# Kernel tuning notes

Measured on AMD Instinct MI355X. Metric: run time of the kernel, lower is better.

The kernel has to match this reference:

```python
import jax, jax.numpy as jnp
import numpy as np

B, S, H = 1, 2048, 2048
NH, NKV, HD = 16, 4, 128
LAT, RD = 512, 64
ND = HD - RD  # nope_dim = 64
EPS = 1e-6


def _rms(x, g):
    return x * jax.lax.rsqrt(jnp.mean(x * x, axis=-1, keepdims=True) + EPS) * g


def _rotate_half(x):
    x1, x2 = jnp.split(x, 2, axis=-1)
    return jnp.concatenate([-x2, x1], axis=-1)


def _rope(x, cos, sin):
    # x: [B,S,nh,RD]; cos/sin: [S,RD] -> broadcast over batch and heads
    c = cos[None, :, None, :]
    s = sin[None, :, None, :]
    return x * c + _rotate_half(x) * s


def setup_inputs() -> dict:
    key = jax.random.key(0)
    ks = jax.random.split(key, 10)
    x = jax.random.normal(ks[0], (B, S, H), jnp.float32)
    # rotary tables (theta=10000) for rope_dim
    inv = 1.0 / (10000.0 ** (np.arange(0, RD, 2, dtype=np.float32) / RD))
    t = np.arange(S, dtype=np.float32)
    freqs = np.outer(t, inv)  # [S, RD/2]
    emb = np.concatenate([freqs, freqs], axis=-1)  # [S, RD]
    cos = jnp.asarray(np.cos(emb), jnp.float32)
    sin = jnp.asarray(np.sin(emb), jnp.float32)
    sc = lambda fan_in: 1.0 / np.sqrt(fan_in)
    Wq_nope = jax.random.normal(ks[1], (NH * ND, H), jnp.float32) * sc(H)
    Wq_rope = jax.random.normal(ks[2], (NH * RD, H), jnp.float32) * sc(H)
    W_kv_down = jax.random.normal(ks[3], (LAT, H), jnp.float32) * sc(H)
    W_k_nope = jax.random.normal(ks[4], (NKV * ND, LAT), jnp.float32) * sc(LAT)
    W_k_rope = jax.random.normal(ks[5], (NKV * RD, LAT), jnp.float32) * sc(LAT)
    W_v = jax.random.normal(ks[6], (NKV * HD, LAT), jnp.float32) * sc(LAT)
    W_o = jax.random.normal(ks[7], (H, NH * HD), jnp.float32) * sc(NH * HD)
    return {
        "x": x, "cos": cos, "sin": sin,
        "Wq_nope": Wq_nope, "Wq_rope": Wq_rope,
        "g_qnope": jnp.ones((ND,), jnp.float32),
        "g_qrope": jnp.ones((RD,), jnp.float32),
        "W_kv_down": W_kv_down, "g_ckv": jnp.ones((LAT,), jnp.float32),
        "W_k_nope": W_k_nope, "W_k_rope": W_k_rope,
        "W_v": W_v, "W_o": W_o,
    }


def reference(x, cos, sin, Wq_nope, Wq_rope, g_qnope, g_qrope,
              W_kv_down, g_ckv, W_k_nope, W_k_rope, W_v, W_o):
    n_rep = NH // NKV
    # queries: decoupled nope / rope parts, RMSNorm each, RoPE on rope part
    q_nope = _rms((x @ Wq_nope.T).reshape(B, S, NH, ND), g_qnope)
    q_rope = _rms((x @ Wq_rope.T).reshape(B, S, NH, RD), g_qrope)
    q_rope = _rope(q_rope, cos[:S, :RD], sin[:S, :RD])
    q = jnp.concatenate([q_nope, q_rope], axis=-1)  # [B,S,NH,HD]
    # latent KV compression
    c_kv = _rms(x @ W_kv_down.T, g_ckv)  # [B,S,LAT]
    k_nope = (c_kv @ W_k_nope.T).reshape(B, S, NKV, ND)
    k_rope = _rope((c_kv @ W_k_rope.T).reshape(B, S, NKV, RD), cos[:S, :RD], sin[:S, :RD])
    v = (c_kv @ W_v.T).reshape(B, S, NKV, HD)
    k = jnp.concatenate([k_nope, k_rope], axis=-1)  # [B,S,NKV,HD]
    # repeat kv heads
    k = jnp.repeat(k, n_rep, axis=2)  # [B,S,NH,HD]
    v = jnp.repeat(v, n_rep, axis=2)
    # causal attention, softmax in fp32
    scores = jnp.einsum("bqhd,bkhd->bhqk", q, k) / jnp.sqrt(jnp.asarray(HD, jnp.float32))
    causal = jnp.tril(jnp.ones((S, S), bool))
    scores = jnp.where(causal[None, None], scores, -jnp.inf)
    attn = jax.nn.softmax(scores.astype(jnp.float32), axis=-1).astype(q.dtype)
    out = jnp.einsum("bhqk,bkhd->bqhd", attn, v).reshape(B, S, NH * HD)
    return out @ W_o.T  # [B,S,H]
```

## Files before the change

### kernel.cpp

```cpp
#include <hip/hip_runtime.h>
#include <hip/hip_bf16.h>
#include <math.h>

#define TPB 256

typedef __attribute__((ext_vector_type(8))) short bf16x8;
typedef __attribute__((ext_vector_type(4))) float f32x4;

__device__ __forceinline__ short f2bs(float x) {
  __hip_bfloat16 h = __float2bfloat16(x);
  return *reinterpret_cast<short*>(&h);
}

__device__ __forceinline__ void gll16(const void* g, void* l) {
  __builtin_amdgcn_global_load_lds(
      (const __attribute__((address_space(1))) unsigned int*)g,
      (__attribute__((address_space(3))) unsigned int*)l, 16, 0, 0);
}

__global__ __launch_bounds__(TPB) void cvt_f2b(
    const float* __restrict__ s, short* __restrict__ d, int n)
{
  int i = (blockIdx.x * TPB + threadIdx.x) << 2;
  if (i >= n) return;
  const float4 v = *(const float4*)(s + i);
  short4 o;
  o.x = f2bs(v.x); o.y = f2bs(v.y); o.z = f2bs(v.z); o.w = f2bs(v.w);
  *(short4*)(d + i) = o;
}

__global__ __launch_bounds__(TPB) void cvt_weights(
    const float* __restrict__ w0, const float* __restrict__ w1,
    const float* __restrict__ w2, const float* __restrict__ w3,
    const float* __restrict__ w4, const float* __restrict__ w5,
    const float* __restrict__ w6,
    short* __restrict__ Wcat, short* __restrict__ Wkvb, short* __restrict__ Wob)
{
  int b = blockIdx.x;
  const float* src; short* dst; int base;
  if (b < 2048)      { src = w0; dst = Wcat;           base = b; }
  else if (b < 4096) { src = w1; dst = Wcat + 2097152; base = b - 2048; }
  else if (b < 5120) { src = w2; dst = Wcat + 4194304; base = b - 4096; }
  else if (b < 5248) { src = w3; dst = Wkvb;           base = b - 5120; }
  else if (b < 5376) { src = w4; dst = Wkvb + 131072;  base = b - 5248; }
  else if (b < 5632) { src = w5; dst = Wkvb + 262144;  base = b - 5376; }
  else               { src = w6; dst = Wob;            base = b - 5632; }
  int i = base * 1024 + threadIdx.x * 4;
  float4 v = *(const float4*)(src + i);
  short4 o;
  o.x = f2bs(v.x); o.y = f2bs(v.y); o.z = f2bs(v.z); o.w = f2bs(v.w);
  *(short4*)(dst + i) = o;
}

__global__ __launch_bounds__(TPB) void rms512b(
    const float* __restrict__ src, short* __restrict__ dst,
    const float* __restrict__ g, int nrows)
{
  int row = blockIdx.x * (TPB / 64) + (threadIdx.x >> 6);
  int l = threadIdx.x & 63;
  if (row >= nrows) return;
  const float* p = src + (size_t)row * 512;
  float x[8];
  float ss = 0.f;
#pragma unroll
  for (int i = 0; i < 8; ++i) { x[i] = p[i * 64 + l]; ss += x[i] * x[i]; }
#pragma unroll
  for (int msk = 1; msk < 64; msk <<= 1) ss += __shfl_xor(ss, msk);
  float r = rsqrtf(ss * (1.0f / 512.0f) + 1e-6f);
#pragma unroll
  for (int i = 0; i < 8; ++i)
    dst[(size_t)row * 512 + i * 64 + l] = f2bs(x[i] * r * g[i * 64 + l]);
}

template <int MODE>
__global__ __launch_bounds__(TPB) void gemm_fused(
    const short* __restrict__ A, const short* __restrict__ W,
    float* __restrict__ Cf, short* __restrict__ qk_out, short* __restrict__ vt,
    float* __restrict__ ckv_f,
    const float* __restrict__ cosb, const float* __restrict__ sinb,
    const float* __restrict__ g_qnope, const float* __restrict__ g_qrope,
    int M, int N, int K, int ldc)
{
  __shared__ short As[2][128 * 64];
  __shared__ short Bs[2][128 * 64];
  const int t = threadIdx.x;
  const int lane = t & 63, wave = t >> 6;
  const int wr = wave >> 1, wc = wave & 1;
  const int li = lane & 15, lh = lane >> 4;
  const int bm = blockIdx.y * 128, bn = blockIdx.x * 128;

  f32x4 acc[4][4];
#pragma unroll
  for (int m = 0; m < 4; ++m)
#pragma unroll
    for (int n = 0; n < 4; ++n) acc[m][n] = (f32x4){0.f, 0.f, 0.f, 0.f};

#define GSTAGE(buf, k0)                                                        \
  {                                                                            \
    _Pragma("unroll") for (int i = 0; i < 4; ++i) {                            \
      int id = i * 256 + t;                                                    \
      int r = id >> 3, cl = id & 7;                                            \
      gll16(A + (size_t)(bm + r) * K + (k0) + ((cl ^ (r & 7)) << 3),           \
            &As[buf][id * 8]);                                                 \
    }                                                                          \
    _Pragma("unroll") for (int i = 0; i < 4; ++i) {                            \
      int id = i * 256 + t;                                                    \
      int r = id >> 3, cl = id & 7;                                            \
      gll16(W + (size_t)(bn + r) * K + (k0) + ((cl ^ (r & 7)) << 3),           \
            &Bs[buf][id * 8]);                                                 \
    }                                                                          \
  }

  GSTAGE(0, 0);
  int cur = 0;
  for (int k0 = 0; k0 < K; k0 += 64) {
    __builtin_amdgcn_sched_barrier(0);
    asm volatile("s_waitcnt lgkmcnt(0)" ::: "memory");
    __builtin_amdgcn_s_barrier();
    __builtin_amdgcn_sched_barrier(0);
    if (k0 + 64 < K) {
      GSTAGE(cur ^ 1, k0 + 64);
      asm volatile("s_waitcnt vmcnt(8)" ::: "memory");
    } else {
      asm volatile("s_waitcnt vmcnt(0)" ::: "memory");
    }
    __builtin_amdgcn_sched_barrier(0);
    bf16x8 af[2][4], bf[2][4];
#pragma unroll
    for (int m = 0; m < 4; ++m) {
      int r = wr * 64 + m * 16 + li;
#pragma unroll
      for (int kd = 0; kd < 2; ++kd)
        af[kd][m] = *(const bf16x8*)&As[cur][r * 64 + (((kd * 4 + lh) ^ (r & 7)) << 3)];
    }
#pragma unroll
    for (int n = 0; n < 4; ++n) {
      int r = wc * 64 + n * 16 + li;
#pragma unroll
      for (int kd = 0; kd < 2; ++kd)
        bf[kd][n] = *(const bf16x8*)&Bs[cur][r * 64 + (((kd * 4 + lh) ^ (r & 7)) << 3)];
    }
    __builtin_amdgcn_s_setprio(1);
#pragma unroll
    for (int kd = 0; kd < 2; ++kd)
#pragma unroll
      for (int m = 0; m < 4; ++m)
#pragma unroll
        for (int n = 0; n < 4; ++n)
          acc[m][n] = __builtin_amdgcn_mfma_f32_16x16x32_bf16(af[kd][m], bf[kd][n],
                                                              acc[m][n], 0, 0, 0);
    __builtin_amdgcn_s_setprio(0);
    __builtin_amdgcn_sched_barrier(0);
    cur ^= 1;
  }
#undef GSTAGE

  const int colbase = bn + wc * 64;

  if (MODE == 0) {
#pragma unroll
    for (int m = 0; m < 4; ++m) {
      int gm = bm + wr * 64 + m * 16 + lh * 4;
#pragma unroll
      for (int n = 0; n < 4; ++n) {
        int gn = colbase + n * 16 + li;
#pragma unroll
        for (int j = 0; j < 4; ++j)
          Cf[(size_t)(gm + j) * ldc + gn] = acc[m][n][j];
      }
    }
  }

  if (MODE == 1) {
    if (colbase < 2048) {
      const bool isrope = colbase >= 1024;
      const int head = (colbase & 1023) >> 6;
      const float* g = isrope ? g_qrope : g_qnope;
      float gv[4];
#pragma unroll
      for (int nf = 0; nf < 4; ++nf) gv[nf] = g[nf * 16 + li];
#pragma unroll
      for (int m = 0; m < 4; ++m) {
#pragma unroll
        for (int j = 0; j < 4; ++j) {
          int s = bm + wr * 64 + m * 16 + lh * 4 + j;
          float sum = acc[m][0][j] * acc[m][0][j] + acc[m][1][j] * acc[m][1][j] +
                      acc[m][2][j] * acc[m][2][j] + acc[m][3][j] * acc[m][3][j];
          sum += __shfl_xor(sum, 1); sum += __shfl_xor(sum, 2);
          sum += __shfl_xor(sum, 4); sum += __shfl_xor(sum, 8);
          float r = rsqrtf(sum * (1.0f / 64.0f) + 1e-6f);
          float y[4];
#pragma unroll
          for (int nf = 0; nf < 4; ++nf) y[nf] = acc[m][nf][j] * r * gv[nf];
          if (isrope) {
            float yr[4];
#pragma unroll
            for (int nf = 0; nf < 4; ++nf) {
              int c = nf * 16 + li;
              float cs = cosb[s * 64 + c], sn = sinb[s * 64 + c];
              float par = (nf < 2) ? -y[nf + 2] : y[nf - 2];
              yr[nf] = y[nf] * cs + par * sn;
            }
#pragma unroll
            for (int nf = 0; nf < 4; ++nf) y[nf] = yr[nf];
          }
#pragma unroll
          for (int nf = 0; nf < 4; ++nf)
            qk_out[(size_t)s * 2048 + head * 128 + (isrope ? 64 : 0) + nf * 16 + li] =
                f2bs(y[nf]);
        }
      }
    } else {
      const int c0 = colbase - 2048;
#pragma unroll
      for (int m = 0; m < 4; ++m) {
        int gm = bm + wr * 64 + m * 16 + lh * 4;
#pragma unroll
        for (int n = 0; n < 4; ++n) {
          int c = c0 + n * 16 + li;
#pragma unroll
          for (int j = 0; j < 4; ++j)
            ckv_f[(size_t)(gm + j) * 512 + c] = acc[m][n][j];
        }
      }
    }
  }

  if (MODE == 2) {
    if (colbase < 512) {
      const bool isrope = colbase >= 256;
      const int kvh = (colbase & 255) >> 6;
#pragma unroll
      for (int m = 0; m < 4; ++m) {
#pragma unroll
        for (int j = 0; j < 4; ++j) {
          int s = bm + wr * 64 + m * 16 + lh * 4 + j;
          float y[4];
#pragma unroll
          for (int nf = 0; nf < 4; ++nf) y[nf] = acc[m][nf][j];
          if (isrope) {
            float yr[4];
#pragma unroll
            for (int nf = 0; nf < 4; ++nf) {
              int c = nf * 16 + li;
              float cs = cosb[s * 64 + c], sn = sinb[s * 64 + c];
              float par = (nf < 2) ? -y[nf + 2] : y[nf - 2];
              yr[nf] = y[nf] * cs + par * sn;
            }
#pragma unroll
            for (int nf = 0; nf < 4; ++nf) y[nf] = yr[nf];
          }
#pragma unroll
          for (int nf = 0; nf < 4; ++nf)
            qk_out[(size_t)s * 512 + kvh * 128 + (isrope ? 64 : 0) + nf * 16 + li] =
                f2bs(y[nf]);
        }
      }
    } else {
#pragma unroll
      for (int m = 0; m < 4; ++m) {
        int s0 = bm + wr * 64 + m * 16 + lh * 4;
#pragma unroll
        for (int nf = 0; nf < 4; ++nf) {
          int d = colbase - 512 + nf * 16 + li;
          int kvh = d >> 7, dd = d & 127;
          short4 pk;
          pk.x = f2bs(acc[m][nf][0]); pk.y = f2bs(acc[m][nf][1]);
          pk.z = f2bs(acc[m][nf][2]); pk.w = f2bs(acc[m][nf][3]);
          *(short4*)&vt[(size_t)kvh * 262144 + (size_t)dd * 2048 + s0] = pk;
        }
      }
    }
  }
}

__global__ __launch_bounds__(TPB) void attn_mfma(
    const short* __restrict__ qb, const short* __restrict__ kb,
    const short* __restrict__ vt, short* __restrict__ ob)
{
  __shared__ short Ks[2][64 * 128];
  __shared__ short Vs[2][128 * 64];
  __shared__ short Ps[4][16 * 64];
  const int h = blockIdx.x;
  const int qt = gridDim.y - 1 - blockIdx.y;
  const int kvh = h >> 2;
  const int t = threadIdx.x, lane = t & 63, wave = t >> 6;
  const int li = lane & 15, lh = lane >> 4;
  const int q0 = qt * 64, q0w = q0 + wave * 16;
  const float scale = 0.08838834764831845f;

  bf16x8 qf[4];
#pragma unroll
  for (int kd = 0; kd < 4; ++kd)
    qf[kd] = *(const bf16x8*)(qb + (size_t)(q0w + li) * 2048 + h * 128 + kd * 32 + lh * 8);

  f32x4 o[8];
#pragma unroll
  for (int n = 0; n < 8; ++n) o[n] = (f32x4){0.f, 0.f, 0.f, 0.f};
  float m_i[4] = {-1e30f, -1e30f, -1e30f, -1e30f};
  float l_i[4] = {0.f, 0.f, 0.f, 0.f};

#define ASTAGE(buf, kbase)                                                     \
  {                                                                            \
    _Pragma("unroll") for (int i = 0; i < 4; ++i) {                            \
      int c = t + i * 256;                                                     \
      int kpos = c >> 4, dcl = (c & 15) ^ (kpos & 7);                          \
      gll16(kb + (size_t)((kbase) + kpos) * 512 + kvh * 128 + dcl * 8,         \
            &Ks[buf][c * 8]);                                                  \
    }                                                                          \
    _Pragma("unroll") for (int i = 0; i < 4; ++i) {                            \
      int c = t + i * 256;                                                     \
      int d = c >> 3, kpl = (c & 7) ^ (d & 7);                                 \
      gll16(vt + (size_t)kvh * 262144 + (size_t)d * 2048 + (kbase) + kpl * 8,  \
            &Vs[buf][c * 8]);                                                  \
    }                                                                          \
  }

  short* pw = Ps[wave];
  const int nkt = qt + 1;
  ASTAGE(0, 0);
  int cur = 0;
  for (int kt = 0; kt < nkt; ++kt) {
    const int kbase = kt * 64;
    __builtin_amdgcn_sched_barrier(0);
    asm volatile("s_waitcnt lgkmcnt(0)" ::: "memory");
    __builtin_amdgcn_s_barrier();
    __builtin_amdgcn_sched_barrier(0);
    if (kt + 1 < nkt) {
      ASTAGE(cur ^ 1, kbase + 64);
      asm volatile("s_waitcnt vmcnt(8)" ::: "memory");
    } else {
      asm volatile("s_waitcnt vmcnt(0)" ::: "memory");
    }
    __builtin_amdgcn_sched_barrier(0);

    f32x4 s[4];
#pragma unroll
    for (int n = 0; n < 4; ++n) s[n] = (f32x4){0.f, 0.f, 0.f, 0.f};
    __builtin_amdgcn_s_setprio(1);
#pragma unroll
    for (int n = 0; n < 4; ++n) {
      int kpos = n * 16 + li;
#pragma unroll
      for (int kd = 0; kd < 4; ++kd) {
        int cph = (kd * 4 + lh) ^ (kpos & 7);
        bf16x8 kf = *(const bf16x8*)&Ks[cur][kpos * 128 + cph * 8];
        s[n] = __builtin_amdgcn_mfma_f32_16x16x32_bf16(qf[kd], kf, s[n], 0, 0, 0);
      }
    }
    __builtin_amdgcn_s_setprio(0);
    float sv[4][4];
    const bool diag = (kt == nkt - 1);
#pragma unroll
    for (int n = 0; n < 4; ++n)
#pragma unroll
      for (int j = 0; j < 4; ++j) {
        float val = s[n][j] * scale;
        if (diag) {
          int kg = kbase + n * 16 + li;
          int qg = q0w + lh * 4 + j;
          if (kg > qg) val = -1e30f;
        }
        sv[n][j] = val;
      }
    float c_[4];
#pragma unroll
    for (int j = 0; j < 4; ++j) {
      float rm = fmaxf(fmaxf(sv[0][j], sv[1][j]), fmaxf(sv[2][j], sv[3][j]));
      rm = fmaxf(rm, __shfl_xor(rm, 1));
      rm = fmaxf(rm, __shfl_xor(rm, 2));
      rm = fmaxf(rm, __shfl_xor(rm, 4));
      rm = fmaxf(rm, __shfl_xor(rm, 8));
      float mn = fmaxf(m_i[j], rm);
      c_[j] = __expf(m_i[j] - mn);
      m_i[j] = mn;
    }
#pragma unroll
    for (int n = 0; n < 4; ++n)
#pragma unroll
      for (int j = 0; j < 4; ++j) sv[n][j] = __expf(sv[n][j] - m_i[j]);
#pragma unroll
    for (int j = 0; j < 4; ++j) {
      float rs = sv[0][j] + sv[1][j] + sv[2][j] + sv[3][j];
      rs += __shfl_xor(rs, 1);
      rs += __shfl_xor(rs, 2);
      rs += __shfl_xor(rs, 4);
      rs += __shfl_xor(rs, 8);
      l_i[j] = l_i[j] * c_[j] + rs;
    }
#pragma unroll
    for (int n = 0; n < 4; ++n)
#pragma unroll
      for (int j = 0; j < 4; ++j) {
        int qq = lh * 4 + j, kp = n * 16 + li;
        pw[qq * 64 + (kp ^ ((qq & 7) << 3))] = f2bs(sv[n][j]);
      }
    if (__any((c_[0] < 1.f) | (c_[1] < 1.f) | (c_[2] < 1.f) | (c_[3] < 1.f))) {
#pragma unroll
      for (int n = 0; n < 8; ++n)
#pragma unroll
        for (int j = 0; j < 4; ++j) o[n][j] *= c_[j];
    }
    asm volatile("s_waitcnt lgkmcnt(0)" ::: "memory");
    __builtin_amdgcn_sched_barrier(0);
    __builtin_amdgcn_s_setprio(1);
#pragma unroll
    for (int kk = 0; kk < 2; ++kk) {
      int kp0 = kk * 32 + lh * 8;
      bf16x8 pf = *(const bf16x8*)&pw[li * 64 + (kp0 ^ ((li & 7) << 3))];
#pragma unroll
      for (int n = 0; n < 8; ++n) {
        int d = n * 16 + li;
        bf16x8 vf = *(const bf16x8*)&Vs[cur][d * 64 + (kp0 ^ ((d & 7) << 3))];
        o[n] = __builtin_amdgcn_mfma_f32_16x16x32_bf16(pf, vf, o[n], 0, 0, 0);
      }
    }
    __builtin_amdgcn_s_setprio(0);
    __builtin_amdgcn_sched_barrier(0);
    cur ^= 1;
  }
#undef ASTAGE
  float inv[4];
#pragma unroll
  for (int j = 0; j < 4; ++j) inv[j] = 1.0f / l_i[j];
#pragma unroll
  for (int n = 0; n < 8; ++n)
#pragma unroll
    for (int j = 0; j < 4; ++j)
      ob[(size_t)(q0w + lh * 4 + j) * 2048 + h * 128 + n * 16 + li] =
          f2bs(o[n][j] * inv[j]);
}

extern "C" void kernel_launch(void* const* d_in, const int* in_sizes, int n_in,
                              void* d_out, int out_size, void* d_ws, size_t ws_size,
                              hipStream_t stream) {
  const float* x         = (const float*)d_in[0];
  const float* cosb      = (const float*)d_in[1];
  const float* sinb      = (const float*)d_in[2];
  const float* Wq_nope   = (const float*)d_in[3];
  const float* Wq_rope   = (const float*)d_in[4];
  const float* g_qnope   = (const float*)d_in[5];
  const float* g_qrope   = (const float*)d_in[6];
  const float* W_kv_down = (const float*)d_in[7];
  const float* g_ckv     = (const float*)d_in[8];
  const float* W_k_nope  = (const float*)d_in[9];
  const float* W_k_rope  = (const float*)d_in[10];
  const float* W_v       = (const float*)d_in[11];
  const float* W_o       = (const float*)d_in[12];
  float* out = (float*)d_out;

  float* ws = (float*)d_ws;
  float* ckv_f = ws;
  short* sb   = (short*)(ws + 1048576);
  short* xb   = sb;
  short* Wcat = sb + 4194304;
  short* Wkvb = Wcat + 5242880;
  short* Wob  = Wkvb + 524288;
  short* qb   = Wob + 4194304;
  short* ckvb = qb + 4194304;
  short* kb   = ckvb + 1048576;
  short* vt   = kb + 1048576;
  short* aob  = xb;

  dim3 blk(TPB);

  cvt_f2b<<<4096, blk, 0, stream>>>(x, xb, 4194304);
  cvt_weights<<<9728, blk, 0, stream>>>(Wq_nope, Wq_rope, W_kv_down, W_k_nope,
                                        W_k_rope, W_v, W_o, Wcat, Wkvb, Wob);

  gemm_fused<1><<<dim3(20, 16), blk, 0, stream>>>(
      xb, Wcat, nullptr, qb, nullptr, ckv_f, cosb, sinb, g_qnope, g_qrope,
      2048, 2560, 2048, 0);

  rms512b<<<512, blk, 0, stream>>>(ckv_f, ckvb, g_ckv, 2048);

  gemm_fused<2><<<dim3(8, 16), blk, 0, stream>>>(
      ckvb, Wkvb, nullptr, kb, vt, nullptr, cosb, sinb, nullptr, nullptr,
      2048, 1024, 512, 0);

  attn_mfma<<<dim3(16, 32), blk, 0, stream>>>(qb, kb, vt, aob);

  gemm_fused<0><<<dim3(16, 16), blk, 0, stream>>>(
      aob, Wob, out, nullptr, nullptr, nullptr, nullptr, nullptr, nullptr, nullptr,
      2048, 2048, 2048, 2048);
}
```

Before: 289.8 us.

## Split-K GEMMs with separate epilogue kernels and 2-wave 32-row attention

All three GEMMs now use split-K across two z-slices, writing fp32 partials that separate epilogue kernels sum while applying RMSNorm, RoPE, the V transpose or the plain output add. The goal is more blocks in flight for the small grids. The attention kernel moves to 128 threads with each wave handling 32 query rows, which reuses each K/V fragment over two MFMA chains and switches to exp2 with a pre-folded scale. In exchange, the split-K partials add extra global memory traffic, and each GEMM needs an extra kernel launch.

After: 349.8 us. 1.21x slower.

```diff
diff --git a/kernel.cpp b/kernel.cpp
--- a/kernel.cpp
+++ b/kernel.cpp
@@ -1,8 +1,6 @@
 #include <hip/hip_runtime.h>
 #include <hip/hip_bf16.h>
 #include <math.h>
-
-#define TPB 256
 
 typedef __attribute__((ext_vector_type(8))) short bf16x8;
 typedef __attribute__((ext_vector_type(4))) float f32x4;
@@ -18,10 +16,10 @@
       (__attribute__((address_space(3))) unsigned int*)l, 16, 0, 0);
 }
 
-__global__ __launch_bounds__(TPB) void cvt_f2b(
+__global__ __launch_bounds__(256) void cvt_f2b(
     const float* __restrict__ s, short* __restrict__ d, int n)
 {
-  int i = (blockIdx.x * TPB + threadIdx.x) << 2;
+  int i = (blockIdx.x * 256 + threadIdx.x) << 2;
   if (i >= n) return;
   const float4 v = *(const float4*)(s + i);
   short4 o;
@@ -29,7 +27,7 @@
   *(short4*)(d + i) = o;
 }
 
-__global__ __launch_bounds__(TPB) void cvt_weights(
+__global__ __launch_bounds__(256) void cvt_weights(
     const float* __restrict__ w0, const float* __restrict__ w1,
     const float* __restrict__ w2, const float* __restrict__ w3,
     const float* __restrict__ w4, const float* __restrict__ w5,
@@ -52,11 +50,11 @@
   *(short4*)(dst + i) = o;
 }
 
-__global__ __launch_bounds__(TPB) void rms512b(
+__global__ __launch_bounds__(256) void rms512b(
     const float* __restrict__ src, short* __restrict__ dst,
     const float* __restrict__ g, int nrows)
 {
-  int row = blockIdx.x * (TPB / 64) + (threadIdx.x >> 6);
+  int row = blockIdx.x * 4 + (threadIdx.x >> 6);
   int l = threadIdx.x & 63;
   if (row >= nrows) return;
   const float* p = src + (size_t)row * 512;
@@ -72,14 +70,9 @@
     dst[(size_t)row * 512 + i * 64 + l] = f2bs(x[i] * r * g[i * 64 + l]);
 }
 
-template <int MODE>
-__global__ __launch_bounds__(TPB) void gemm_fused(
+__global__ __launch_bounds__(256) void gemm_ks(
     const short* __restrict__ A, const short* __restrict__ W,
-    float* __restrict__ Cf, short* __restrict__ qk_out, short* __restrict__ vt,
-    float* __restrict__ ckv_f,
-    const float* __restrict__ cosb, const float* __restrict__ sinb,
-    const float* __restrict__ g_qnope, const float* __restrict__ g_qrope,
-    int M, int N, int K, int ldc)
+    float* __restrict__ C, int M, int N, int K, int KH)
 {
   __shared__ short As[2][128 * 64];
   __shared__ short Bs[2][128 * 64];
@@ -88,6 +81,8 @@
   const int wr = wave >> 1, wc = wave & 1;
   const int li = lane & 15, lh = lane >> 4;
   const int bm = blockIdx.y * 128, bn = blockIdx.x * 128;
+  const int zoff = blockIdx.z * KH;
+  float* Cp = C + (size_t)blockIdx.z * M * N;
 
   f32x4 acc[4][4];
 #pragma unroll
@@ -100,25 +95,25 @@
     _Pragma("unroll") for (int i = 0; i < 4; ++i) {                            \
       int id = i * 256 + t;                                                    \
       int r = id >> 3, cl = id & 7;                                            \
-      gll16(A + (size_t)(bm + r) * K + (k0) + ((cl ^ (r & 7)) << 3),           \
+      gll16(A + (size_t)(bm + r) * K + zoff + (k0) + ((cl ^ (r & 7)) << 3),    \
             &As[buf][id * 8]);                                                 \
     }                                                                          \
     _Pragma("unroll") for (int i = 0; i < 4; ++i) {                            \
       int id = i * 256 + t;                                                    \
       int r = id >> 3, cl = id & 7;                                            \
-      gll16(W + (size_t)(bn + r) * K + (k0) + ((cl ^ (r & 7)) << 3),           \
+      gll16(W + (size_t)(bn + r) * K + zoff + (k0) + ((cl ^ (r & 7)) << 3),    \
             &Bs[buf][id * 8]);                                                 \
     }                                                                          \
   }
 
   GSTAGE(0, 0);
   int cur = 0;
-  for (int k0 = 0; k0 < K; k0 += 64) {
+  for (int k0 = 0; k0 < KH; k0 += 64) {
     __builtin_amdgcn_sched_barrier(0);
     asm volatile("s_waitcnt lgkmcnt(0)" ::: "memory");
     __builtin_amdgcn_s_barrier();
     __builtin_amdgcn_sched_barrier(0);
-    if (k0 + 64 < K) {
+    if (k0 + 64 < KH) {
       GSTAGE(cur ^ 1, k0 + 64);
       asm volatile("s_waitcnt vmcnt(8)" ::: "memory");
     } else {
@@ -155,161 +150,148 @@
   }
 #undef GSTAGE
 
-  const int colbase = bn + wc * 64;
-
-  if (MODE == 0) {
-#pragma unroll
-    for (int m = 0; m < 4; ++m) {
-      int gm = bm + wr * 64 + m * 16 + lh * 4;
-#pragma unroll
-      for (int n = 0; n < 4; ++n) {
-        int gn = colbase + n * 16 + li;
-#pragma unroll
-        for (int j = 0; j < 4; ++j)
-          Cf[(size_t)(gm + j) * ldc + gn] = acc[m][n][j];
-      }
-    }
-  }
-
-  if (MODE == 1) {
-    if (colbase < 2048) {
-      const bool isrope = colbase >= 1024;
-      const int head = (colbase & 1023) >> 6;
-      const float* g = isrope ? g_qrope : g_qnope;
-      float gv[4];
-#pragma unroll
-      for (int nf = 0; nf < 4; ++nf) gv[nf] = g[nf * 16 + li];
-#pragma unroll
-      for (int m = 0; m < 4; ++m) {
-#pragma unroll
-        for (int j = 0; j < 4; ++j) {
-          int s = bm + wr * 64 + m * 16 + lh * 4 + j;
-          float sum = acc[m][0][j] * acc[m][0][j] + acc[m][1][j] * acc[m][1][j] +
-                      acc[m][2][j] * acc[m][2][j] + acc[m][3][j] * acc[m][3][j];
-          sum += __shfl_xor(sum, 1); sum += __shfl_xor(sum, 2);
-          sum += __shfl_xor(sum, 4); sum += __shfl_xor(sum, 8);
-          float r = rsqrtf(sum * (1.0f / 64.0f) + 1e-6f);
-          float y[4];
-#pragma unroll
-          for (int nf = 0; nf < 4; ++nf) y[nf] = acc[m][nf][j] * r * gv[nf];
-          if (isrope) {
-            float yr[4];
-#pragma unroll
-            for (int nf = 0; nf < 4; ++nf) {
-              int c = nf * 16 + li;
-              float cs = cosb[s * 64 + c], sn = sinb[s * 64 + c];
-              float par = (nf < 2) ? -y[nf + 2] : y[nf - 2];
-              yr[nf] = y[nf] * cs + par * sn;
-            }
-#pragma unroll
-            for (int nf = 0; nf < 4; ++nf) y[nf] = yr[nf];
-          }
-#pragma unroll
-          for (int nf = 0; nf < 4; ++nf)
-            qk_out[(size_t)s * 2048 + head * 128 + (isrope ? 64 : 0) + nf * 16 + li] =
-                f2bs(y[nf]);
-        }
-      }
-    } else {
-      const int c0 = colbase - 2048;
-#pragma unroll
-      for (int m = 0; m < 4; ++m) {
-        int gm = bm + wr * 64 + m * 16 + lh * 4;
-#pragma unroll
-        for (int n = 0; n < 4; ++n) {
-          int c = c0 + n * 16 + li;
-#pragma unroll
-          for (int j = 0; j < 4; ++j)
-            ckv_f[(size_t)(gm + j) * 512 + c] = acc[m][n][j];
-        }
-      }
-    }
-  }
-
-  if (MODE == 2) {
-    if (colbase < 512) {
-      const bool isrope = colbase >= 256;
-      const int kvh = (colbase & 255) >> 6;
-#pragma unroll
-      for (int m = 0; m < 4; ++m) {
-#pragma unroll
-        for (int j = 0; j < 4; ++j) {
-          int s = bm + wr * 64 + m * 16 + lh * 4 + j;
-          float y[4];
-#pragma unroll
-          for (int nf = 0; nf < 4; ++nf) y[nf] = acc[m][nf][j];
-          if (isrope) {
-            float yr[4];
-#pragma unroll
-            for (int nf = 0; nf < 4; ++nf) {
-              int c = nf * 16 + li;
-              float cs = cosb[s * 64 + c], sn = sinb[s * 64 + c];
-              float par = (nf < 2) ? -y[nf + 2] : y[nf - 2];
-              yr[nf] = y[nf] * cs + par * sn;
-            }
-#pragma unroll
-            for (int nf = 0; nf < 4; ++nf) y[nf] = yr[nf];
-          }
-#pragma unroll
-          for (int nf = 0; nf < 4; ++nf)
-            qk_out[(size_t)s * 512 + kvh * 128 + (isrope ? 64 : 0) + nf * 16 + li] =
-                f2bs(y[nf]);
-        }
-      }
-    } else {
-#pragma unroll
-      for (int m = 0; m < 4; ++m) {
-        int s0 = bm + wr * 64 + m * 16 + lh * 4;
-#pragma unroll
-        for (int nf = 0; nf < 4; ++nf) {
-          int d = colbase - 512 + nf * 16 + li;
-          int kvh = d >> 7, dd = d & 127;
-          short4 pk;
-          pk.x = f2bs(acc[m][nf][0]); pk.y = f2bs(acc[m][nf][1]);
-          pk.z = f2bs(acc[m][nf][2]); pk.w = f2bs(acc[m][nf][3]);
-          *(short4*)&vt[(size_t)kvh * 262144 + (size_t)dd * 2048 + s0] = pk;
-        }
-      }
-    }
-  }
-}
-
-__global__ __launch_bounds__(TPB) void attn_mfma(
+#pragma unroll
+  for (int m = 0; m < 4; ++m) {
+    int gm = bm + wr * 64 + m * 16 + lh * 4;
+#pragma unroll
+    for (int n = 0; n < 4; ++n) {
+      int gn = bn + wc * 64 + n * 16 + li;
+#pragma unroll
+      for (int j = 0; j < 4; ++j)
+        Cp[(size_t)(gm + j) * N + gn] = acc[m][n][j];
+    }
+  }
+}
+
+__global__ __launch_bounds__(256) void ep_q(
+    const float* __restrict__ P0, const float* __restrict__ P1,
+    short* __restrict__ qb, float* __restrict__ ckv_f,
+    const float* __restrict__ cosb, const float* __restrict__ sinb,
+    const float* __restrict__ g_qnope, const float* __restrict__ g_qrope)
+{
+  const int r = blockIdx.y;
+  const int cg = blockIdx.x * 4 + (threadIdx.x >> 6);
+  const int l = threadIdx.x & 63;
+  const int n = cg * 64 + l;
+  float val = P0[(size_t)r * 2560 + n] + P1[(size_t)r * 2560 + n];
+  if (cg >= 32) {
+    ckv_f[(size_t)r * 512 + (n - 2048)] = val;
+    return;
+  }
+  const bool rope = cg >= 16;
+  float ss = val * val;
+#pragma unroll
+  for (int msk = 1; msk < 64; msk <<= 1) ss += __shfl_xor(ss, msk);
+  float rr = rsqrtf(ss * (1.0f / 64.0f) + 1e-6f);
+  float y = val * rr * (rope ? g_qrope[l] : g_qnope[l]);
+  if (rope) {
+    float partner = __shfl_xor(y, 32);
+    float c = cosb[r * 64 + l], sn = sinb[r * 64 + l];
+    y = y * c + ((l < 32) ? -partner : partner) * sn;
+  }
+  const int head = cg & 15;
+  qb[(size_t)r * 2048 + head * 128 + (rope ? 64 : 0) + l] = f2bs(y);
+}
+
+__global__ __launch_bounds__(256) void ep_kv(
+    const float* __restrict__ P0, const float* __restrict__ P1,
+    short* __restrict__ kb,
+    const float* __restrict__ cosb, const float* __restrict__ sinb)
+{
+  const int r = blockIdx.y;
+  const int cg = blockIdx.x * 4 + (threadIdx.x >> 6);
+  const int l = threadIdx.x & 63;
+  const int n = cg * 64 + l;
+  float y = P0[(size_t)r * 1024 + n] + P1[(size_t)r * 1024 + n];
+  const bool rope = cg >= 4;
+  if (rope) {
+    float partner = __shfl_xor(y, 32);
+    float c = cosb[r * 64 + l], sn = sinb[r * 64 + l];
+    y = y * c + ((l < 32) ? -partner : partner) * sn;
+  }
+  const int kvh = cg & 3;
+  kb[(size_t)r * 512 + kvh * 128 + (rope ? 64 : 0) + l] = f2bs(y);
+}
+
+__global__ __launch_bounds__(256) void ep_vt(
+    const float* __restrict__ P0, const float* __restrict__ P1,
+    short* __restrict__ vt)
+{
+  __shared__ float tile[64][65];
+  const int st = blockIdx.x, dh = blockIdx.y, kvh = blockIdx.z;
+  const int r4 = threadIdx.x >> 6, cl = threadIdx.x & 63;
+  const int col = 512 + kvh * 128 + dh * 64 + cl;
+#pragma unroll
+  for (int i = 0; i < 16; ++i) {
+    int srow = i * 4 + r4;
+    size_t idx = (size_t)(st * 64 + srow) * 1024 + col;
+    tile[srow][cl] = P0[idx] + P1[idx];
+  }
+  __syncthreads();
+#pragma unroll
+  for (int i = 0; i < 16; ++i) {
+    int drow = i * 4 + r4;
+    vt[(size_t)kvh * 262144 + (size_t)(dh * 64 + drow) * 2048 + st * 64 + cl] =
+        f2bs(tile[cl][drow]);
+  }
+}
+
+__global__ __launch_bounds__(256) void ep_out(
+    const float* __restrict__ P0, const float* __restrict__ P1,
+    float* __restrict__ out)
+{
+  int i = (blockIdx.x * 256 + threadIdx.x) << 2;
+  float4 a = *(const float4*)(P0 + i);
+  float4 b = *(const float4*)(P1 + i);
+  float4 o;
+  o.x = a.x + b.x; o.y = a.y + b.y; o.z = a.z + b.z; o.w = a.w + b.w;
+  *(float4*)(out + i) = o;
+}
+
+__global__ __launch_bounds__(128) void attn_mfma(
     const short* __restrict__ qb, const short* __restrict__ kb,
     const short* __restrict__ vt, short* __restrict__ ob)
 {
   __shared__ short Ks[2][64 * 128];
   __shared__ short Vs[2][128 * 64];
-  __shared__ short Ps[4][16 * 64];
+  __shared__ short Ps[2][32 * 64];
   const int h = blockIdx.x;
   const int qt = gridDim.y - 1 - blockIdx.y;
   const int kvh = h >> 2;
   const int t = threadIdx.x, lane = t & 63, wave = t >> 6;
   const int li = lane & 15, lh = lane >> 4;
-  const int q0 = qt * 64, q0w = q0 + wave * 16;
-  const float scale = 0.08838834764831845f;
-
-  bf16x8 qf[4];
-#pragma unroll
-  for (int kd = 0; kd < 4; ++kd)
-    qf[kd] = *(const bf16x8*)(qb + (size_t)(q0w + li) * 2048 + h * 128 + kd * 32 + lh * 8);
-
-  f32x4 o[8];
-#pragma unroll
-  for (int n = 0; n < 8; ++n) o[n] = (f32x4){0.f, 0.f, 0.f, 0.f};
-  float m_i[4] = {-1e30f, -1e30f, -1e30f, -1e30f};
-  float l_i[4] = {0.f, 0.f, 0.f, 0.f};
+  const int q0 = qt * 64, q0w = q0 + wave * 32;
+  const float sc2 = 0.08838834764831845f * 1.44269504088896f;
+
+  bf16x8 qf[2][4];
+#pragma unroll
+  for (int rf = 0; rf < 2; ++rf)
+#pragma unroll
+    for (int kd = 0; kd < 4; ++kd)
+      qf[rf][kd] = *(const bf16x8*)(qb + (size_t)(q0w + rf * 16 + li) * 2048 +
+                                    h * 128 + kd * 32 + lh * 8);
+
+  f32x4 o[2][8];
+#pragma unroll
+  for (int rf = 0; rf < 2; ++rf)
+#pragma unroll
+    for (int n = 0; n < 8; ++n) o[rf][n] = (f32x4){0.f, 0.f, 0.f, 0.f};
+  float m_i[2][4], l_i[2][4];
+#pragma unroll
+  for (int rf = 0; rf < 2; ++rf)
+#pragma unroll
+    for (int j = 0; j < 4; ++j) { m_i[rf][j] = -1e30f; l_i[rf][j] = 0.f; }
 
 #define ASTAGE(buf, kbase)                                                     \
   {                                                                            \
-    _Pragma("unroll") for (int i = 0; i < 4; ++i) {                            \
-      int c = t + i * 256;                                                     \
+    _Pragma("unroll") for (int i = 0; i < 8; ++i) {                            \
+      int c = t + i * 128;                                                     \
       int kpos = c >> 4, dcl = (c & 15) ^ (kpos & 7);                          \
       gll16(kb + (size_t)((kbase) + kpos) * 512 + kvh * 128 + dcl * 8,         \
             &Ks[buf][c * 8]);                                                  \
     }                                                                          \
-    _Pragma("unroll") for (int i = 0; i < 4; ++i) {                            \
-      int c = t + i * 256;                                                     \
+    _Pragma("unroll") for (int i = 0; i < 8; ++i) {                            \
+      int c = t + i * 128;                                                     \
       int d = c >> 3, kpl = (c & 7) ^ (d & 7);                                 \
       gll16(vt + (size_t)kvh * 262144 + (size_t)d * 2048 + (kbase) + kpl * 8,  \
             &Vs[buf][c * 8]);                                                  \
@@ -328,15 +310,17 @@
     __builtin_amdgcn_sched_barrier(0);
     if (kt + 1 < nkt) {
       ASTAGE(cur ^ 1, kbase + 64);
-      asm volatile("s_waitcnt vmcnt(8)" ::: "memory");
+      asm volatile("s_waitcnt vmcnt(16)" ::: "memory");
     } else {
       asm volatile("s_waitcnt vmcnt(0)" ::: "memory");
     }
     __builtin_amdgcn_sched_barrier(0);
 
-    f32x4 s[4];
-#pragma unroll
-    for (int n = 0; n < 4; ++n) s[n] = (f32x4){0.f, 0.f, 0.f, 0.f};
+    f32x4 s[2][4];
+#pragma unroll
+    for (int rf = 0; rf < 2; ++rf)
+#pragma unroll
+      for (int n = 0; n < 4; ++n) s[rf][n] = (f32x4){0.f, 0.f, 0.f, 0.f};
     __builtin_amdgcn_s_setprio(1);
 #pragma unroll
     for (int n = 0; n < 4; ++n) {
@@ -345,61 +329,77 @@
       for (int kd = 0; kd < 4; ++kd) {
         int cph = (kd * 4 + lh) ^ (kpos & 7);
         bf16x8 kf = *(const bf16x8*)&Ks[cur][kpos * 128 + cph * 8];
-        s[n] = __builtin_amdgcn_mfma_f32_16x16x32_bf16(qf[kd], kf, s[n], 0, 0, 0);
+        s[0][n] = __builtin_amdgcn_mfma_f32_16x16x32_bf16(qf[0][kd], kf, s[0][n], 0, 0, 0);
+        s[1][n] = __builtin_amdgcn_mfma_f32_16x16x32_bf16(qf[1][kd], kf, s[1][n], 0, 0, 0);
       }
     }
     __builtin_amdgcn_s_setprio(0);
-    float sv[4][4];
-    const bool diag = (kt == nkt - 1);
-#pragma unroll
-    for (int n = 0; n < 4; ++n)
+    float sv[2][4][4];
+    const bool dg = (kbase + 63 > q0w);
+#pragma unroll
+    for (int rf = 0; rf < 2; ++rf)
+#pragma unroll
+      for (int n = 0; n < 4; ++n)
+#pragma unroll
+        for (int j = 0; j < 4; ++j) {
+          float val = s[rf][n][j] * sc2;
+          if (dg) {
+            int kg = kbase + n * 16 + li;
+            int qg = q0w + rf * 16 + lh * 4 + j;
+            if (kg > qg) val = -1e30f;
+          }
+          sv[rf][n][j] = val;
+        }
+    float c_[2][4];
+    float cmin = 1.f;
+#pragma unroll
+    for (int rf = 0; rf < 2; ++rf)
 #pragma unroll
       for (int j = 0; j < 4; ++j) {
-        float val = s[n][j] * scale;
-        if (diag) {
-          int kg = kbase + n * 16 + li;
-          int qg = q0w + lh * 4 + j;
-          if (kg > qg) val = -1e30f;
+        float rm = fmaxf(fmaxf(sv[rf][0][j], sv[rf][1][j]),
+                         fmaxf(sv[rf][2][j], sv[rf][3][j]));
+        rm = fmaxf(rm, __shfl_xor(rm, 1));
+        rm = fmaxf(rm, __shfl_xor(rm, 2));
+        rm = fmaxf(rm, __shfl_xor(rm, 4));
+        rm = fmaxf(rm, __shfl_xor(rm, 8));
+        float mn = fmaxf(m_i[rf][j], rm);
+        c_[rf][j] = exp2f(m_i[rf][j] - mn);
+        m_i[rf][j] = mn;
+        cmin = fminf(cmin, c_[rf][j]);
+      }
+#pragma unroll
+    for (int rf = 0; rf < 2; ++rf)
+#pragma unroll
+      for (int n = 0; n < 4; ++n)
+#pragma unroll
+        for (int j = 0; j < 4; ++j) sv[rf][n][j] = exp2f(sv[rf][n][j] - m_i[rf][j]);
+#pragma unroll
+    for (int rf = 0; rf < 2; ++rf)
+#pragma unroll
+      for (int j = 0; j < 4; ++j) {
+        float rs = sv[rf][0][j] + sv[rf][1][j] + sv[rf][2][j] + sv[rf][3][j];
+        rs += __shfl_xor(rs, 1);
+        rs += __shfl_xor(rs, 2);
+        rs += __shfl_xor(rs, 4);
+        rs += __shfl_xor(rs, 8);
+        l_i[rf][j] = l_i[rf][j] * c_[rf][j] + rs;
+      }
+#pragma unroll
+    for (int rf = 0; rf < 2; ++rf)
+#pragma unroll
+      for (int n = 0; n < 4; ++n)
+#pragma unroll
+        for (int j = 0; j < 4; ++j) {
+          int qq = rf * 16 + lh * 4 + j, kp = n * 16 + li;
+          pw[qq * 64 + (kp ^ ((qq & 7) << 3))] = f2bs(sv[rf][n][j]);
         }
-        sv[n][j] = val;
-      }
-    float c_[4];
-#pragma unroll
-    for (int j = 0; j < 4; ++j) {
-      float rm = fmaxf(fmaxf(sv[0][j], sv[1][j]), fmaxf(sv[2][j], sv[3][j]));
-      rm = fmaxf(rm, __shfl_xor(rm, 1));
-      rm = fmaxf(rm, __shfl_xor(rm, 2));
-      rm = fmaxf(rm, __shfl_xor(rm, 4));
-      rm = fmaxf(rm, __shfl_xor(rm, 8));
-      float mn = fmaxf(m_i[j], rm);
-      c_[j] = __expf(m_i[j] - mn);
-      m_i[j] = mn;
-    }
-#pragma unroll
-    for (int n = 0; n < 4; ++n)
-#pragma unroll
-      for (int j = 0; j < 4; ++j) sv[n][j] = __expf(sv[n][j] - m_i[j]);
-#pragma unroll
-    for (int j = 0; j < 4; ++j) {
-      float rs = sv[0][j] + sv[1][j] + sv[2][j] + sv[3][j];
-      rs += __shfl_xor(rs, 1);
-      rs += __shfl_xor(rs, 2);
-      rs += __shfl_xor(rs, 4);
-      rs += __shfl_xor(rs, 8);
-      l_i[j] = l_i[j] * c_[j] + rs;
-    }
-#pragma unroll
-    for (int n = 0; n < 4; ++n)
-#pragma unroll
-      for (int j = 0; j < 4; ++j) {
-        int qq = lh * 4 + j, kp = n * 16 + li;
-        pw[qq * 64 + (kp ^ ((qq & 7) << 3))] = f2bs(sv[n][j]);
-      }
-    if (__any((c_[0] < 1.f) | (c_[1] < 1.f) | (c_[2] < 1.f) | (c_[3] < 1.f))) {
-#pragma unroll
-      for (int n = 0; n < 8; ++n)
-#pragma unroll
-        for (int j = 0; j < 4; ++j) o[n][j] *= c_[j];
+    if (__any(cmin < 1.f)) {
+#pragma unroll
+      for (int rf = 0; rf < 2; ++rf)
+#pragma unroll
+        for (int n = 0; n < 8; ++n)
+#pragma unroll
+          for (int j = 0; j < 4; ++j) o[rf][n][j] *= c_[rf][j];
     }
     asm volatile("s_waitcnt lgkmcnt(0)" ::: "memory");
     __builtin_amdgcn_sched_barrier(0);
@@ -407,12 +407,14 @@
 #pragma unroll
     for (int kk = 0; kk < 2; ++kk) {
       int kp0 = kk * 32 + lh * 8;
-      bf16x8 pf = *(const bf16x8*)&pw[li * 64 + (kp0 ^ ((li & 7) << 3))];
+      bf16x8 pf0 = *(const bf16x8*)&pw[li * 64 + (kp0 ^ ((li & 7) << 3))];
+      bf16x8 pf1 = *(const bf16x8*)&pw[(16 + li) * 64 + (kp0 ^ ((li & 7) << 3))];
 #pragma unroll
       for (int n = 0; n < 8; ++n) {
         int d = n * 16 + li;
         bf16x8 vf = *(const bf16x8*)&Vs[cur][d * 64 + (kp0 ^ ((d & 7) << 3))];
-        o[n] = __builtin_amdgcn_mfma_f32_16x16x32_bf16(pf, vf, o[n], 0, 0, 0);
+        o[0][n] = __builtin_amdgcn_mfma_f32_16x16x32_bf16(pf0, vf, o[0][n], 0, 0, 0);
+        o[1][n] = __builtin_amdgcn_mfma_f32_16x16x32_bf16(pf1, vf, o[1][n], 0, 0, 0);
       }
     }
     __builtin_amdgcn_s_setprio(0);
@@ -420,15 +422,18 @@
     cur ^= 1;
   }
 #undef ASTAGE
-  float inv[4];
-#pragma unroll
-  for (int j = 0; j < 4; ++j) inv[j] = 1.0f / l_i[j];
-#pragma unroll
-  for (int n = 0; n < 8; ++n)
-#pragma unroll
-    for (int j = 0; j < 4; ++j)
-      ob[(size_t)(q0w + lh * 4 + j) * 2048 + h * 128 + n * 16 + li] =
-          f2bs(o[n][j] * inv[j]);
+#pragma unroll
+  for (int rf = 0; rf < 2; ++rf) {
+    float inv[4];
+#pragma unroll
+    for (int j = 0; j < 4; ++j) inv[j] = 1.0f / l_i[rf][j];
+#pragma unroll
+    for (int n = 0; n < 8; ++n)
+#pragma unroll
+      for (int j = 0; j < 4; ++j)
+        ob[(size_t)(q0w + rf * 16 + lh * 4 + j) * 2048 + h * 128 + n * 16 + li] =
+            f2bs(o[rf][n][j] * inv[j]);
+  }
 }
 
 extern "C" void kernel_launch(void* const* d_in, const int* in_sizes, int n_in,
@@ -450,37 +455,41 @@
   float* out = (float*)d_out;
 
   float* ws = (float*)d_ws;
-  float* ckv_f = ws;
-  short* sb   = (short*)(ws + 1048576);
+  float* Pq0 = ws;
+  float* Pq1 = ws + 5242880;
+  float* Po0 = ws;
+  float* Po1 = ws + 4194304;
+  float* ckv_f = ws + 10485760;
+  short* sb = (short*)(ws + 11534336);
   short* xb   = sb;
   short* Wcat = sb + 4194304;
-  short* Wkvb = Wcat + 5242880;
-  short* Wob  = Wkvb + 524288;
-  short* qb   = Wob + 4194304;
-  short* ckvb = qb + 4194304;
-  short* kb   = ckvb + 1048576;
-  short* vt   = kb + 1048576;
-  short* aob  = xb;
-
-  dim3 blk(TPB);
+  float* Pkv0 = (float*)sb;
+  float* Pkv1 = (float*)sb + 2097152;
+  short* aob  = sb;
+  short* Wkvb = sb + 9437184;
+  short* Wob  = sb + 9961472;
+  short* qb   = sb + 14155776;
+  short* ckvb = sb + 18350080;
+  short* kb   = sb + 19398656;
+  short* vt   = sb + 20447232;
+
+  dim3 blk(256);
 
   cvt_f2b<<<4096, blk, 0, stream>>>(x, xb, 4194304);
   cvt_weights<<<9728, blk, 0, stream>>>(Wq_nope, Wq_rope, W_kv_down, W_k_nope,
                                         W_k_rope, W_v, W_o, Wcat, Wkvb, Wob);
 
-  gemm_fused<1><<<dim3(20, 16), blk, 0, stream>>>(
-      xb, Wcat, nullptr, qb, nullptr, ckv_f, cosb, sinb, g_qnope, g_qrope,
-      2048, 2560, 2048, 0);
-
+  gemm_ks<<<dim3(20, 16, 2), blk, 0, stream>>>(xb, Wcat, Pq0, 2048, 2560, 2048, 1024);
+  ep_q<<<dim3(10, 2048), blk, 0, stream>>>(Pq0, Pq1, qb, ckv_f, cosb, sinb,
+                                           g_qnope, g_qrope);
   rms512b<<<512, blk, 0, stream>>>(ckv_f, ckvb, g_ckv, 2048);
 
-  gemm_fused<2><<<dim3(8, 16), blk, 0, stream>>>(
-      ckvb, Wkvb, nullptr, kb, vt, nullptr, cosb, sinb, nullptr, nullptr,
-      2048, 1024, 512, 0);
-
-  attn_mfma<<<dim3(16, 32), blk, 0, stream>>>(qb, kb, vt, aob);
-
-  gemm_fused<0><<<dim3(16, 16), blk, 0, stream>>>(
-      aob, Wob, out, nullptr, nullptr, nullptr, nullptr, nullptr, nullptr, nullptr,
-      2048, 2048, 2048, 2048);
-}
+  gemm_ks<<<dim3(8, 16, 2), blk, 0, stream>>>(ckvb, Wkvb, Pkv0, 2048, 1024, 512, 256);
+  ep_kv<<<dim3(2, 2048), blk, 0, stream>>>(Pkv0, Pkv1, kb, cosb, sinb);
+  ep_vt<<<dim3(32, 2, 4), blk, 0, stream>>>(Pkv0, Pkv1, vt);
+
+  attn_mfma<<<dim3(16, 32), dim3(128), 0, stream>>>(qb, kb, vt, aob);
+
+  gemm_ks<<<dim3(16, 16, 2), blk, 0, stream>>>(aob, Wob, Po0, 2048, 2048, 2048, 1024);
+  ep_out<<<4096, blk, 0, stream>>>(Po0, Po1, out);
+}
```
